# Optimization experiments

Measured on AMD Instinct MI355X. Metric: run time of the kernel, lower is better.

The kernel has to match this reference:

```python
import jax, jax.numpy as jnp
import numpy as np

N, D, H = 4096, 128, 8


def setup_inputs() -> dict:
    key = jax.random.key(0)
    ks = jax.random.split(key, 9)
    s = 1.0 / np.sqrt(D)
    return {
        "x": jax.random.normal(ks[0], (N, D), jnp.float32),
        "Wq": jax.random.normal(ks[1], (H, D, D), jnp.float32) * s,
        "bq": jax.random.normal(ks[2], (H, D), jnp.float32) * s,
        "Wk": jax.random.normal(ks[3], (H, D, D), jnp.float32) * s,
        "bk": jax.random.normal(ks[4], (H, D), jnp.float32) * s,
        "Wv": jax.random.normal(ks[5], (H, D, D), jnp.float32) * s,
        "bv": jax.random.normal(ks[6], (H, D), jnp.float32) * s,
        "Wo": jax.random.normal(ks[7], (H * D, D), jnp.float32) * s,
        "bo": jax.random.normal(ks[8], (D,), jnp.float32) * s,
    }


def reference(x, Wq, bq, Wk, bk, Wv, bv, Wo, bo):
    # Batched per-head projections: [H, N, D]
    q = jnp.einsum('nd,hde->hne', x, Wq) + bq[:, None, :]
    k = jnp.einsum('nd,hde->hne', x, Wk) + bk[:, None, :]
    v = jnp.einsum('nd,hde->hne', x, Wv) + bv[:, None, :]
    # Non-standard attention: scores = v @ q.T  -> [H, N, N]
    scores = jnp.einsum('hnd,hmd->hnm', v, q)
    wts = jax.nn.softmax(scores, axis=-1)
    out = jnp.einsum('hnm,hmd->hnd', wts, k)  # [H, N, D]
    # Concat heads along feature dim (head-major order, as torch.cat)
    outs = out.transpose(1, 0, 2).reshape(N, H * D)
    return outs @ Wo + bo
```

## Files before the change

kernel.cpp:

```cpp
#include <hip/hip_runtime.h>
#include <hip/hip_bf16.h>


typedef __attribute__((ext_vector_type(8))) short short8;
typedef __attribute__((ext_vector_type(4))) float f32x4;

#define MFMA(a,b,c) __builtin_amdgcn_mfma_f32_16x16x32_bf16((a),(b),(c),0,0,0)
#define LOG2E 1.44269504088896340736f
#define DEFER_THR 8.0f

#define AS1 __attribute__((address_space(1)))
#define AS3 __attribute__((address_space(3)))
static __device__ __forceinline__ void gld16(const void* g, void* l) {
  __builtin_amdgcn_global_load_lds((const AS1 void*)g, (AS3 void*)l, 16, 0, 0);
}

static __device__ __forceinline__ unsigned short f2bf(float f) {
  union { float f; unsigned u; } v; v.f = f;
  unsigned r = v.u + 0x7fffu + ((v.u >> 16) & 1u);
  return (unsigned short)(r >> 16);
}
static __device__ __forceinline__ float bf2f(unsigned short h) {
  union { unsigned u; float f; } v; v.u = ((unsigned)h) << 16; return v.f;
}
static __device__ __forceinline__ void split2(float f, unsigned short& hi, unsigned short& lo) {
  hi = f2bf(f);
  lo = f2bf(f - bf2f(hi));
}

__global__ __launch_bounds__(256) void kwt(const float* __restrict__ Wq,
                                           const float* __restrict__ Wk,
                                           const float* __restrict__ Wv,
                                           const float* __restrict__ Wo,
                                           unsigned short* __restrict__ WTh,
                                           unsigned short* __restrict__ WTl,
                                           unsigned short* __restrict__ WoT) {
  __shared__ float lds[64 * 130];
  int b = blockIdx.x, t = threadIdx.x;
  const float* src; int isWo;
  if (b < 24) {
    int slot = b >> 3, hh = b & 7;
    src = (slot == 0 ? Wq : (slot == 1 ? Wk : Wv)) + hh * 16384;
    isWo = 0;
  } else {
    src = Wo + (b - 24) * 16384;
    isWo = 1;
  }
  for (int half = 0; half < 2; ++half) {
#pragma unroll
    for (int i = 0; i < 8; ++i) {
      int lin = i * 1024 + t * 4;
      int row = lin >> 7, col = lin & 127;
      float4 v = *reinterpret_cast<const float4*>(src + half * 8192 + lin);
      lds[row * 130 + col + 0] = v.x;
      lds[row * 130 + col + 1] = v.y;
      lds[row * 130 + col + 2] = v.z;
      lds[row * 130 + col + 3] = v.w;
    }
    __syncthreads();
    int e = t >> 1, k0 = (t & 1) * 32;
    float buf[32];
#pragma unroll
    for (int j = 0; j < 32; ++j) buf[j] = lds[(k0 + j) * 130 + e];
    int kg = half * 64 + k0;
    if (!isWo) {
      unsigned short* dh = WTh + b * 16384 + e * 128 + kg;
      unsigned short* dl = WTl + b * 16384 + e * 128 + kg;
#pragma unroll
      for (int c = 0; c < 4; ++c) {
        short8 oh, ol;
#pragma unroll
        for (int jj = 0; jj < 8; ++jj) {
          unsigned short h, l; split2(buf[c * 8 + jj], h, l);
          oh[jj] = (short)h; ol[jj] = (short)l;
        }
        *reinterpret_cast<short8*>(dh + c * 8) = oh;
        *reinterpret_cast<short8*>(dl + c * 8) = ol;
      }
    } else {
      unsigned short* dst = WoT + e * 1024 + (b - 24) * 128 + kg;
#pragma unroll
      for (int c = 0; c < 4; ++c) {
        short8 o;
#pragma unroll
        for (int jj = 0; jj < 8; ++jj) o[jj] = (short)f2bf(buf[c * 8 + jj]);
        *reinterpret_cast<short8*>(dst + c * 8) = o;
      }
    }
    __syncthreads();
  }
}

__global__ __launch_bounds__(256) void kprojf(const float* __restrict__ x,
                                              const unsigned short* __restrict__ WThg,
                                              const unsigned short* __restrict__ WTlg,
                                              const float* __restrict__ bq,
                                              const float* __restrict__ bk,
                                              const float* __restrict__ bv,
                                              unsigned short* __restrict__ Qh,
                                              unsigned short* __restrict__ Vh,
                                              unsigned short* __restrict__ Vl,
                                              unsigned short* __restrict__ Kt) {
  __shared__ __align__(16) unsigned char lds[64 * 128 * 2];
  int nb = blockIdx.x, h = blockIdx.y;
  int t = threadIdx.x, lane = t & 63, w = t >> 6;
  int r = lane & 15, g = lane >> 4;
  int rowbase = nb * 64 + w * 16;

  short8 ah[4], al[4];
#pragma unroll
  for (int kc = 0; kc < 4; ++kc) {
    const float* xp = x + (size_t)(rowbase + r) * 128 + kc * 32 + g * 8;
    float4 f0 = *reinterpret_cast<const float4*>(xp);
    float4 f1 = *reinterpret_cast<const float4*>(xp + 4);
    unsigned short hi_, lo_;
    split2(f0.x, hi_, lo_); ah[kc][0] = (short)hi_; al[kc][0] = (short)lo_;
    split2(f0.y, hi_, lo_); ah[kc][1] = (short)hi_; al[kc][1] = (short)lo_;
    split2(f0.z, hi_, lo_); ah[kc][2] = (short)hi_; al[kc][2] = (short)lo_;
    split2(f0.w, hi_, lo_); ah[kc][3] = (short)hi_; al[kc][3] = (short)lo_;
    split2(f1.x, hi_, lo_); ah[kc][4] = (short)hi_; al[kc][4] = (short)lo_;
    split2(f1.y, hi_, lo_); ah[kc][5] = (short)hi_; al[kc][5] = (short)lo_;
    split2(f1.z, hi_, lo_); ah[kc][6] = (short)hi_; al[kc][6] = (short)lo_;
    split2(f1.w, hi_, lo_); ah[kc][7] = (short)hi_; al[kc][7] = (short)lo_;
  }

  f32x4 acc[8];
  {
    const unsigned short* Wth = WThg + (0 * 8 + h) * 16384;
    const unsigned short* Wtl = WTlg + (0 * 8 + h) * 16384;
#pragma unroll
    for (int ct = 0; ct < 8; ++ct) acc[ct] = (f32x4){0.f, 0.f, 0.f, 0.f};
#pragma unroll
    for (int ct = 0; ct < 8; ++ct) {
#pragma unroll
      for (int kc = 0; kc < 4; ++kc) {
        short8 bh = *reinterpret_cast<const short8*>(Wth + (ct * 16 + r) * 128 + kc * 32 + g * 8);
        short8 bl = *reinterpret_cast<const short8*>(Wtl + (ct * 16 + r) * 128 + kc * 32 + g * 8);
        acc[ct] = MFMA(ah[kc], bh, acc[ct]);
        acc[ct] = MFMA(ah[kc], bl, acc[ct]);
        acc[ct] = MFMA(al[kc], bh, acc[ct]);
      }
    }
    unsigned short* dh = Qh + (size_t)h * 4096 * 128;
#pragma unroll
    for (int ct = 0; ct < 8; ++ct) {
      int e = ct * 16 + r;
      float bb = bq[h * 128 + e];
#pragma unroll
      for (int rr = 0; rr < 4; ++rr) {
        int n = rowbase + g * 4 + rr;
        dh[n * 128 + e] = f2bf(acc[ct][rr] + bb);
      }
    }
  }
  {
    const unsigned short* Wth = WThg + (2 * 8 + h) * 16384;
    const unsigned short* Wtl = WTlg + (2 * 8 + h) * 16384;
#pragma unroll
    for (int ct = 0; ct < 8; ++ct) acc[ct] = (f32x4){0.f, 0.f, 0.f, 0.f};
#pragma unroll
    for (int ct = 0; ct < 8; ++ct) {
#pragma unroll
      for (int kc = 0; kc < 4; ++kc) {
        short8 bh = *reinterpret_cast<const short8*>(Wth + (ct * 16 + r) * 128 + kc * 32 + g * 8);
        short8 bl = *reinterpret_cast<const short8*>(Wtl + (ct * 16 + r) * 128 + kc * 32 + g * 8);
        acc[ct] = MFMA(ah[kc], bh, acc[ct]);
        acc[ct] = MFMA(ah[kc], bl, acc[ct]);
        acc[ct] = MFMA(al[kc], bh, acc[ct]);
      }
    }
    unsigned short* dh = Vh + (size_t)h * 4096 * 128;
    unsigned short* dl = Vl + (size_t)h * 4096 * 128;
#pragma unroll
    for (int ct = 0; ct < 8; ++ct) {
      int e = ct * 16 + r;
      float bb = bv[h * 128 + e];
#pragma unroll
      for (int rr = 0; rr < 4; ++rr) {
        int n = rowbase + g * 4 + rr;
        unsigned short hi_, lo_; split2(acc[ct][rr] + bb, hi_, lo_);
        dh[n * 128 + e] = hi_;
        dl[n * 128 + e] = lo_;
      }
    }
  }
  {
    const unsigned short* Wth = WThg + (1 * 8 + h) * 16384;
#pragma unroll
    for (int ct = 0; ct < 8; ++ct) acc[ct] = (f32x4){0.f, 0.f, 0.f, 0.f};
#pragma unroll
    for (int ct = 0; ct < 8; ++ct) {
#pragma unroll
      for (int kc = 0; kc < 4; ++kc) {
        short8 bh = *reinterpret_cast<const short8*>(Wth + (ct * 16 + r) * 128 + kc * 32 + g * 8);
        acc[ct] = MFMA(ah[kc], bh, acc[ct]);
      }
    }
#pragma unroll
    for (int ct = 0; ct < 8; ++ct) {
      int e = ct * 16 + r;
      float bb = bk[h * 128 + e];
#pragma unroll
      for (int rr = 0; rr < 4; ++rr) {
        int n = w * 16 + g * 4 + rr;
        unsigned off = ((unsigned)(n * 128 + e) * 2u) ^ ((unsigned)(n & 7) << 4);
        *reinterpret_cast<unsigned short*>(lds + off) = f2bf(acc[ct][rr] + bb);
      }
    }
    __syncthreads();
    int e = t >> 1, n0 = (t & 1) * 32;
    unsigned short buf[32];
#pragma unroll
    for (int j = 0; j < 32; ++j) {
      int n = n0 + j;
      unsigned off = ((unsigned)(n * 128 + e) * 2u) ^ ((unsigned)(n & 7) << 4);
      buf[j] = *reinterpret_cast<unsigned short*>(lds + off);
    }
    unsigned short* dst = Kt + ((size_t)h * 128 + e) * 4096 + nb * 64 + n0;
#pragma unroll
    for (int c = 0; c < 4; ++c) {
      short8 o;
#pragma unroll
      for (int jj = 0; jj < 8; ++jj) o[jj] = (short)buf[c * 8 + jj];
      *reinterpret_cast<short8*>(dst + c * 8) = o;
    }
  }
}

__global__ __launch_bounds__(128, 2) void kattn(
    const unsigned short* __restrict__ Qg,
    const unsigned short* __restrict__ Kt,
    const unsigned short* __restrict__ Vh,
    const unsigned short* __restrict__ Vl,
    unsigned short* __restrict__ Opart,
    float2* __restrict__ ml) {
  __shared__ __align__(16) unsigned char qlds[2][8192];
  __shared__ __align__(16) unsigned char klds[2][8192];
  __shared__ __align__(16) unsigned short plds[2][32 * 40];
  const int h = blockIdx.x, nb = blockIdx.y, z = blockIdx.z;
  const int t = threadIdx.x, lane = t & 63, w = t >> 6;
  const int r = lane & 15, g = lane >> 4;
  const unsigned char* Qb = (const unsigned char*)(Qg + (size_t)h * 4096 * 128);
  const unsigned char* Kb = (const unsigned char*)(Kt + (size_t)h * 128 * 4096);

  const int vbase = nb * 64 + w * 32;
  short8 va0h[4], va0l[4], va1h[4], va1l[4];
#pragma unroll
  for (int kc = 0; kc < 4; ++kc) {
    size_t o0 = (size_t)h * 4096 * 128 + (size_t)(vbase + r) * 128 + kc * 32 + g * 8;
    size_t o1 = (size_t)h * 4096 * 128 + (size_t)(vbase + 16 + r) * 128 + kc * 32 + g * 8;
    va0h[kc] = *reinterpret_cast<const short8*>(Vh + o0);
    va0l[kc] = *reinterpret_cast<const short8*>(Vl + o0);
    va1h[kc] = *reinterpret_cast<const short8*>(Vh + o1);
    va1l[kc] = *reinterpret_cast<const short8*>(Vl + o1);
  }

  f32x4 oacc0[8], oacc1[8];
#pragma unroll
  for (int dt = 0; dt < 8; ++dt) {
    oacc0[dt] = (f32x4){0.f, 0.f, 0.f, 0.f};
    oacc1[dt] = (f32x4){0.f, 0.f, 0.f, 0.f};
  }
  float m0run = -3e38f, l0run = 0.f, m1run = -3e38f, l1run = 0.f;
  const int mt0 = z * 64;

#define STAGE(buf, mtile) do {                                                   \
    const unsigned char* qsrc = Qb + (size_t)(mtile) * 8192;                     \
    const unsigned char* ksrc = Kb + (size_t)(mtile) * 64;                       \
    _Pragma("unroll")                                                            \
    for (int j = 0; j < 4; ++j) {                                                \
      int row = j * 8 + (t >> 4);                                                \
      gld16(qsrc + (size_t)row * 256 + (((unsigned)(t & 15) * 16) ^ ((unsigned)(row & 7) << 4)), \
            &qlds[buf][j * 2048 + t * 16]);                                      \
    }                                                                            \
    _Pragma("unroll")                                                            \
    for (int j = 0; j < 4; ++j) {                                                \
      int row = j * 32 + (t >> 2);                                               \
      gld16(ksrc + (size_t)row * 8192 + (unsigned)(t & 3) * 16,                  \
            &klds[buf][j * 2048 + t * 16]);                                      \
    }                                                                            \
  } while (0)

  STAGE(0, mt0);
  __syncthreads();

  const unsigned qsw = ((unsigned)(r & 7)) << 4;
  for (int it = 0; it < 64; ++it) {
    const int buf = it & 1;
    if (it < 63) STAGE(buf ^ 1, mt0 + it + 1);
    f32x4 s00 = (f32x4){0.f, 0.f, 0.f, 0.f};
    f32x4 s10 = (f32x4){0.f, 0.f, 0.f, 0.f};
    f32x4 s01 = (f32x4){0.f, 0.f, 0.f, 0.f};
    f32x4 s11 = (f32x4){0.f, 0.f, 0.f, 0.f};
    __builtin_amdgcn_s_setprio(1);
#pragma unroll
    for (int kc = 0; kc < 4; ++kc) {
      unsigned col = (unsigned)(kc * 64 + g * 16);
      short8 q0 = *reinterpret_cast<const short8*>(&qlds[buf][(unsigned)r * 256 + (col ^ qsw)]);
      short8 q1 = *reinterpret_cast<const short8*>(&qlds[buf][(unsigned)(16 + r) * 256 + (col ^ qsw)]);
      s00 = MFMA(q0, va0h[kc], s00);
      s10 = MFMA(q1, va0h[kc], s10);
      s01 = MFMA(q0, va1h[kc], s01);
      s11 = MFMA(q1, va1h[kc], s11);
      s00 = MFMA(q0, va0l[kc], s00);
      s10 = MFMA(q1, va0l[kc], s10);
      s01 = MFMA(q0, va1l[kc], s01);
      s11 = MFMA(q1, va1l[kc], s11);
    }
    __builtin_amdgcn_s_setprio(0);
    float mx0 = fmaxf(fmaxf(fmaxf(s00[0], s00[1]), fmaxf(s00[2], s00[3])),
                      fmaxf(fmaxf(s10[0], s10[1]), fmaxf(s10[2], s10[3])));
    float mx1 = fmaxf(fmaxf(fmaxf(s01[0], s01[1]), fmaxf(s01[2], s01[3])),
                      fmaxf(fmaxf(s11[0], s11[1]), fmaxf(s11[2], s11[3])));
    mx0 = fmaxf(mx0, __shfl_xor(mx0, 16)); mx0 = fmaxf(mx0, __shfl_xor(mx0, 32));
    mx1 = fmaxf(mx1, __shfl_xor(mx1, 16)); mx1 = fmaxf(mx1, __shfl_xor(mx1, 32));
    if (__any(mx0 > m0run + DEFER_THR)) {
      float nm = fmaxf(m0run, mx0);
      float sc = exp2f((m0run - nm) * LOG2E);
      l0run *= sc;
#pragma unroll
      for (int dt = 0; dt < 8; ++dt) oacc0[dt] *= sc;
      m0run = nm;
    }
    if (__any(mx1 > m1run + DEFER_THR)) {
      float nm = fmaxf(m1run, mx1);
      float sc = exp2f((m1run - nm) * LOG2E);
      l1run *= sc;
#pragma unroll
      for (int dt = 0; dt < 8; ++dt) oacc1[dt] *= sc;
      m1run = nm;
    }
    float p0[8], p1[8];
#pragma unroll
    for (int j = 0; j < 4; ++j) {
      p0[j]     = exp2f((s00[j] - m0run) * LOG2E);
      p0[4 + j] = exp2f((s10[j] - m0run) * LOG2E);
      p1[j]     = exp2f((s01[j] - m1run) * LOG2E);
      p1[4 + j] = exp2f((s11[j] - m1run) * LOG2E);
    }
    float ps0 = ((p0[0] + p0[1]) + (p0[2] + p0[3])) + ((p0[4] + p0[5]) + (p0[6] + p0[7]));
    float ps1 = ((p1[0] + p1[1]) + (p1[2] + p1[3])) + ((p1[4] + p1[5]) + (p1[6] + p1[7]));
    ps0 += __shfl_xor(ps0, 16); ps0 += __shfl_xor(ps0, 32);
    ps1 += __shfl_xor(ps1, 16); ps1 += __shfl_xor(ps1, 32);
    l0run += ps0;
    l1run += ps1;
    {
      ushort4 a, b, c, d;
      a.x = f2bf(p0[0]); a.y = f2bf(p0[1]); a.z = f2bf(p0[2]); a.w = f2bf(p0[3]);
      b.x = f2bf(p0[4]); b.y = f2bf(p0[5]); b.z = f2bf(p0[6]); b.w = f2bf(p0[7]);
      c.x = f2bf(p1[0]); c.y = f2bf(p1[1]); c.z = f2bf(p1[2]); c.w = f2bf(p1[3]);
      d.x = f2bf(p1[4]); d.y = f2bf(p1[5]); d.z = f2bf(p1[6]); d.w = f2bf(p1[7]);
      unsigned short* pw = &plds[w][0];
      *reinterpret_cast<ushort4*>(pw + r * 40 + g * 4)             = a;
      *reinterpret_cast<ushort4*>(pw + r * 40 + 16 + g * 4)        = b;
      *reinterpret_cast<ushort4*>(pw + (16 + r) * 40 + g * 4)      = c;
      *reinterpret_cast<ushort4*>(pw + (16 + r) * 40 + 16 + g * 4) = d;
    }
    short8 pa0 = *reinterpret_cast<const short8*>(&plds[w][r * 40 + g * 8]);
    short8 pa1 = *reinterpret_cast<const short8*>(&plds[w][(16 + r) * 40 + g * 8]);
    __builtin_amdgcn_s_setprio(1);
#pragma unroll
    for (int dt = 0; dt < 8; ++dt) {
      short8 kb = *reinterpret_cast<const short8*>(&klds[buf][(unsigned)(dt * 16 + r) * 64 + (unsigned)(g * 16)]);
      oacc0[dt] = MFMA(kb, pa0, oacc0[dt]);
      oacc1[dt] = MFMA(kb, pa1, oacc1[dt]);
    }
    __builtin_amdgcn_s_setprio(0);
    __syncthreads();
  }
#undef STAGE
  unsigned short* Ob = Opart + (size_t)(z * 8 + h) * 4096 * 128;
#pragma unroll
  for (int dt = 0; dt < 8; ++dt) {
#pragma unroll
    for (int rr = 0; rr < 4; ++rr) {
      int d = dt * 16 + g * 4 + rr;
      Ob[(size_t)(vbase + r) * 128 + d]      = f2bf(oacc0[dt][rr]);
      Ob[(size_t)(vbase + 16 + r) * 128 + d] = f2bf(oacc1[dt][rr]);
    }
  }
  if (g == 0) ml[(size_t)(z * 8 + h) * 4096 + vbase + r]      = make_float2(m0run, l0run);
  if (g == 1) ml[(size_t)(z * 8 + h) * 4096 + vbase + 16 + r] = make_float2(m1run, l1run);
}

__global__ __launch_bounds__(256) void koutm(const unsigned short* __restrict__ Opart,
                                             const float2* __restrict__ ml,
                                             const unsigned short* __restrict__ WoT,
                                             const float* __restrict__ bo,
                                             float* __restrict__ out) {
  int rb = blockIdx.x;
  int t = threadIdx.x, lane = t & 63, w = t >> 6;
  int r = lane & 15, g = lane >> 4;
  int row = rb * 16 + r;
  float a0[8], a1[8];
#pragma unroll
  for (int h = 0; h < 8; ++h) {
    float2 m0 = ml[(size_t)h * 4096 + row];
    float2 m1 = ml[(size_t)(8 + h) * 4096 + row];
    float M = fmaxf(m0.x, m1.x);
    float e0 = exp2f((m0.x - M) * LOG2E);
    float e1 = exp2f((m1.x - M) * LOG2E);
    float inv = 1.0f / (m0.y * e0 + m1.y * e1);
    a0[h] = e0 * inv; a1[h] = e1 * inv;
  }
  f32x4 acc0 = (f32x4){0.f, 0.f, 0.f, 0.f};
  f32x4 acc1 = (f32x4){0.f, 0.f, 0.f, 0.f};
#pragma unroll
  for (int kc = 0; kc < 32; ++kc) {
    int h = kc >> 2;
    int dof = (kc & 3) * 32 + g * 8;
    short8 o0 = *reinterpret_cast<const short8*>(Opart + ((size_t)h * 4096 + row) * 128 + dof);
    short8 o1 = *reinterpret_cast<const short8*>(Opart + ((size_t)(8 + h) * 4096 + row) * 128 + dof);
    short8 af;
#pragma unroll
    for (int j = 0; j < 8; ++j)
      af[j] = (short)f2bf(bf2f((unsigned short)o0[j]) * a0[h] +
                          bf2f((unsigned short)o1[j]) * a1[h]);
    short8 b0 = *reinterpret_cast<const short8*>(WoT + (size_t)(w * 32 + r) * 1024 + kc * 32 + g * 8);
    short8 b1 = *reinterpret_cast<const short8*>(WoT + (size_t)(w * 32 + 16 + r) * 1024 + kc * 32 + g * 8);
    acc0 = MFMA(af, b0, acc0);
    acc1 = MFMA(af, b1, acc1);
  }
#pragma unroll
  for (int rr = 0; rr < 4; ++rr) {
    int n = rb * 16 + g * 4 + rr;
    out[(size_t)n * 128 + w * 32 + r]      = acc0[rr] + bo[w * 32 + r];
    out[(size_t)n * 128 + w * 32 + 16 + r] = acc1[rr] + bo[w * 32 + 16 + r];
  }
}

extern "C" void kernel_launch(void* const* d_in, const int* in_sizes, int n_in,
                              void* d_out, int out_size, void* d_ws, size_t ws_size,
                              hipStream_t stream) {
  const float* x  = (const float*)d_in[0];
  const float* Wq = (const float*)d_in[1];
  const float* bq = (const float*)d_in[2];
  const float* Wk = (const float*)d_in[3];
  const float* bk = (const float*)d_in[4];
  const float* Wv = (const float*)d_in[5];
  const float* bv = (const float*)d_in[6];
  const float* Wo = (const float*)d_in[7];
  const float* bo = (const float*)d_in[8];
  float* out = (float*)d_out;

  unsigned short* ws = (unsigned short*)d_ws;
  unsigned short* WTh   = ws;
  unsigned short* WTl   = WTh + 393216;
  unsigned short* WoT   = WTl + 393216;
  unsigned short* Qh    = WoT + 131072;
  unsigned short* Vh    = Qh + 4194304;
  unsigned short* Vl    = Vh + 4194304;
  unsigned short* Kt    = Vl + 4194304;
  unsigned short* Opart = Kt + 4194304;
  float2*         mlp   = (float2*)(Opart + 8388608);

  kwt<<<32, 256, 0, stream>>>(Wq, Wk, Wv, Wo, WTh, WTl, WoT);
  kprojf<<<dim3(64, 8), 256, 0, stream>>>(x, WTh, WTl, bq, bk, bv, Qh, Vh, Vl, Kt);
  kattn<<<dim3(8, 64, 2), 128, 0, stream>>>(Qh, Kt, Vh, Vl, Opart, mlp);
  koutm<<<256, 256, 0, stream>>>(Opart, mlp, WoT, bo, out);
}
```

Before: 275.4 us.

## Rework attention split, register P exchange, log2 prescale, and wider kernel grids

The attention kernel now runs 256-thread blocks covering 128 query rows and splits keys four ways instead of two. The P tile is packed to bf16 and rearranged with cross-lane shuffles instead of a round trip through LDS, and the K tile in LDS is XOR-swizzled. V is pre-multiplied by log2(e) so the exponentials drop a multiply, with the deferred-rescale threshold adjusted to match. The weight-transpose and output kernels are split over more blocks, and the output kernel combines four partial results using packed bf16 conversion. The wider split adds partial-output traffic and merge work, and the raised occupancy target may increase register pressure.

```diff
diff --git a/kernel.cpp b/kernel.cpp
--- a/kernel.cpp
+++ b/kernel.cpp
@@ -7,7 +7,7 @@
 
 #define MFMA(a,b,c) __builtin_amdgcn_mfma_f32_16x16x32_bf16((a),(b),(c),0,0,0)
 #define LOG2E 1.44269504088896340736f
-#define DEFER_THR 8.0f
+#define DEFER_THR 11.5442f
 
 #define AS1 __attribute__((address_space(1)))
 #define AS3 __attribute__((address_space(3)))
@@ -26,6 +26,32 @@
 static __device__ __forceinline__ void split2(float f, unsigned short& hi, unsigned short& lo) {
   hi = f2bf(f);
   lo = f2bf(f - bf2f(hi));
+}
+static __device__ __forceinline__ unsigned cvt_pk_bf16(float lo, float hi) {
+  unsigned r;
+  asm("v_cvt_pk_bf16_f32 %0, %1, %2" : "=v"(r) : "v"(lo), "v"(hi));
+  return r;
+}
+
+static __device__ __forceinline__ void pexch(const float* p, int lane, unsigned* t) {
+  unsigned A = cvt_pk_bf16(p[0], p[1]);
+  unsigned B = cvt_pk_bf16(p[2], p[3]);
+  unsigned C = cvt_pk_bf16(p[4], p[5]);
+  unsigned D = cvt_pk_bf16(p[6], p[7]);
+  bool lo32 = (lane & 32) == 0;
+  unsigned A32 = __shfl_xor(A, 32), B32 = __shfl_xor(B, 32);
+  unsigned C32 = __shfl_xor(C, 32), D32 = __shfl_xor(D, 32);
+  unsigned u0 = lo32 ? A : C32;
+  unsigned u1 = lo32 ? A32 : C;
+  unsigned v0 = lo32 ? B : D32;
+  unsigned v1 = lo32 ? B32 : D;
+  bool eg = (lane & 16) == 0;
+  unsigned su1 = __shfl_xor(u1, 16), su0 = __shfl_xor(u0, 16);
+  unsigned sv1 = __shfl_xor(v1, 16), sv0 = __shfl_xor(v0, 16);
+  t[0] = eg ? u0 : su1;
+  t[1] = eg ? v0 : sv1;
+  t[2] = eg ? su0 : u1;
+  t[3] = eg ? sv0 : v1;
 }
 
 __global__ __launch_bounds__(256) void kwt(const float* __restrict__ Wq,
@@ -35,59 +61,53 @@
                                            unsigned short* __restrict__ WTh,
                                            unsigned short* __restrict__ WTl,
                                            unsigned short* __restrict__ WoT) {
-  __shared__ float lds[64 * 130];
+  __shared__ float lds[32 * 130];
   int b = blockIdx.x, t = threadIdx.x;
-  const float* src; int isWo;
-  if (b < 24) {
-    int slot = b >> 3, hh = b & 7;
-    src = (slot == 0 ? Wq : (slot == 1 ? Wk : Wv)) + hh * 16384;
-    isWo = 0;
+  int mat = b >> 2, q = b & 3;
+  const float* src = (mat < 8)  ? Wq + mat * 16384
+                   : (mat < 16) ? Wk + (mat - 8) * 16384
+                   : (mat < 24) ? Wv + (mat - 16) * 16384
+                                : Wo + (mat - 24) * 16384;
+  src += q * 32 * 128;
+#pragma unroll
+  for (int i = 0; i < 4; ++i) {
+    int lin = i * 1024 + t * 4;
+    int row = lin >> 7, col = lin & 127;
+    float4 v = *reinterpret_cast<const float4*>(src + lin);
+    lds[row * 130 + col + 0] = v.x;
+    lds[row * 130 + col + 1] = v.y;
+    lds[row * 130 + col + 2] = v.z;
+    lds[row * 130 + col + 3] = v.w;
+  }
+  __syncthreads();
+  int e = t >> 1, ks = (t & 1) * 16;
+  float buf[16];
+#pragma unroll
+  for (int j = 0; j < 16; ++j) buf[j] = lds[(ks + j) * 130 + e];
+  int kg = q * 32 + ks;
+  if (mat < 24) {
+    unsigned short* dh = WTh + mat * 16384 + e * 128 + kg;
+    unsigned short* dl = WTl + mat * 16384 + e * 128 + kg;
+#pragma unroll
+    for (int c = 0; c < 2; ++c) {
+      short8 oh, ol;
+#pragma unroll
+      for (int jj = 0; jj < 8; ++jj) {
+        unsigned short h, l; split2(buf[c * 8 + jj], h, l);
+        oh[jj] = (short)h; ol[jj] = (short)l;
+      }
+      *reinterpret_cast<short8*>(dh + c * 8) = oh;
+      *reinterpret_cast<short8*>(dl + c * 8) = ol;
+    }
   } else {
-    src = Wo + (b - 24) * 16384;
-    isWo = 1;
-  }
-  for (int half = 0; half < 2; ++half) {
-#pragma unroll
-    for (int i = 0; i < 8; ++i) {
-      int lin = i * 1024 + t * 4;
-      int row = lin >> 7, col = lin & 127;
-      float4 v = *reinterpret_cast<const float4*>(src + half * 8192 + lin);
-      lds[row * 130 + col + 0] = v.x;
-      lds[row * 130 + col + 1] = v.y;
-      lds[row * 130 + col + 2] = v.z;
-      lds[row * 130 + col + 3] = v.w;
-    }
-    __syncthreads();
-    int e = t >> 1, k0 = (t & 1) * 32;
-    float buf[32];
-#pragma unroll
-    for (int j = 0; j < 32; ++j) buf[j] = lds[(k0 + j) * 130 + e];
-    int kg = half * 64 + k0;
-    if (!isWo) {
-      unsigned short* dh = WTh + b * 16384 + e * 128 + kg;
-      unsigned short* dl = WTl + b * 16384 + e * 128 + kg;
-#pragma unroll
-      for (int c = 0; c < 4; ++c) {
-        short8 oh, ol;
-#pragma unroll
-        for (int jj = 0; jj < 8; ++jj) {
-          unsigned short h, l; split2(buf[c * 8 + jj], h, l);
-          oh[jj] = (short)h; ol[jj] = (short)l;
-        }
-        *reinterpret_cast<short8*>(dh + c * 8) = oh;
-        *reinterpret_cast<short8*>(dl + c * 8) = ol;
-      }
-    } else {
-      unsigned short* dst = WoT + e * 1024 + (b - 24) * 128 + kg;
-#pragma unroll
-      for (int c = 0; c < 4; ++c) {
-        short8 o;
-#pragma unroll
-        for (int jj = 0; jj < 8; ++jj) o[jj] = (short)f2bf(buf[c * 8 + jj]);
-        *reinterpret_cast<short8*>(dst + c * 8) = o;
-      }
-    }
-    __syncthreads();
+    unsigned short* dst = WoT + e * 1024 + (mat - 24) * 128 + kg;
+#pragma unroll
+    for (int c = 0; c < 2; ++c) {
+      short8 o;
+#pragma unroll
+      for (int jj = 0; jj < 8; ++jj) o[jj] = (short)f2bf(buf[c * 8 + jj]);
+      *reinterpret_cast<short8*>(dst + c * 8) = o;
+    }
   }
 }
 
@@ -178,7 +198,7 @@
 #pragma unroll
       for (int rr = 0; rr < 4; ++rr) {
         int n = rowbase + g * 4 + rr;
-        unsigned short hi_, lo_; split2(acc[ct][rr] + bb, hi_, lo_);
+        unsigned short hi_, lo_; split2((acc[ct][rr] + bb) * LOG2E, hi_, lo_);
         dh[n * 128 + e] = hi_;
         dl[n * 128 + e] = lo_;
       }
@@ -227,7 +247,7 @@
   }
 }
 
-__global__ __launch_bounds__(128, 2) void kattn(
+__global__ __launch_bounds__(256, 3) void kattn(
     const unsigned short* __restrict__ Qg,
     const unsigned short* __restrict__ Kt,
     const unsigned short* __restrict__ Vh,
@@ -236,14 +256,13 @@
     float2* __restrict__ ml) {
   __shared__ __align__(16) unsigned char qlds[2][8192];
   __shared__ __align__(16) unsigned char klds[2][8192];
-  __shared__ __align__(16) unsigned short plds[2][32 * 40];
   const int h = blockIdx.x, nb = blockIdx.y, z = blockIdx.z;
   const int t = threadIdx.x, lane = t & 63, w = t >> 6;
   const int r = lane & 15, g = lane >> 4;
   const unsigned char* Qb = (const unsigned char*)(Qg + (size_t)h * 4096 * 128);
   const unsigned char* Kb = (const unsigned char*)(Kt + (size_t)h * 128 * 4096);
 
-  const int vbase = nb * 64 + w * 32;
+  const int vbase = nb * 128 + w * 32;
   short8 va0h[4], va0l[4], va1h[4], va1l[4];
 #pragma unroll
   for (int kc = 0; kc < 4; ++kc) {
@@ -262,22 +281,23 @@
     oacc1[dt] = (f32x4){0.f, 0.f, 0.f, 0.f};
   }
   float m0run = -3e38f, l0run = 0.f, m1run = -3e38f, l1run = 0.f;
-  const int mt0 = z * 64;
+  const int mt0 = z * 32;
 
 #define STAGE(buf, mtile) do {                                                   \
     const unsigned char* qsrc = Qb + (size_t)(mtile) * 8192;                     \
     const unsigned char* ksrc = Kb + (size_t)(mtile) * 64;                       \
     _Pragma("unroll")                                                            \
-    for (int j = 0; j < 4; ++j) {                                                \
-      int row = j * 8 + (t >> 4);                                                \
+    for (int j = 0; j < 2; ++j) {                                                \
+      int row = j * 16 + (t >> 4);                                               \
       gld16(qsrc + (size_t)row * 256 + (((unsigned)(t & 15) * 16) ^ ((unsigned)(row & 7) << 4)), \
-            &qlds[buf][j * 2048 + t * 16]);                                      \
+            &qlds[buf][j * 4096 + t * 16]);                                      \
     }                                                                            \
     _Pragma("unroll")                                                            \
-    for (int j = 0; j < 4; ++j) {                                                \
-      int row = j * 32 + (t >> 2);                                               \
-      gld16(ksrc + (size_t)row * 8192 + (unsigned)(t & 3) * 16,                  \
-            &klds[buf][j * 2048 + t * 16]);                                      \
+    for (int j = 0; j < 2; ++j) {                                                \
+      int d = j * 64 + (t >> 2);                                                 \
+      int c = (t & 3) ^ (d & 3);                                                 \
+      gld16(ksrc + (size_t)d * 8192 + (unsigned)c * 16,                          \
+            &klds[buf][j * 4096 + t * 16]);                                      \
     }                                                                            \
   } while (0)
 
@@ -285,9 +305,10 @@
   __syncthreads();
 
   const unsigned qsw = ((unsigned)(r & 7)) << 4;
-  for (int it = 0; it < 64; ++it) {
+  const unsigned kxor = ((unsigned)(g ^ (r & 3))) << 4;
+  for (int it = 0; it < 32; ++it) {
     const int buf = it & 1;
-    if (it < 63) STAGE(buf ^ 1, mt0 + it + 1);
+    if (it < 31) STAGE(buf ^ 1, mt0 + it + 1);
     f32x4 s00 = (f32x4){0.f, 0.f, 0.f, 0.f};
     f32x4 s10 = (f32x4){0.f, 0.f, 0.f, 0.f};
     f32x4 s01 = (f32x4){0.f, 0.f, 0.f, 0.f};
@@ -316,7 +337,7 @@
     mx1 = fmaxf(mx1, __shfl_xor(mx1, 16)); mx1 = fmaxf(mx1, __shfl_xor(mx1, 32));
     if (__any(mx0 > m0run + DEFER_THR)) {
       float nm = fmaxf(m0run, mx0);
-      float sc = exp2f((m0run - nm) * LOG2E);
+      float sc = exp2f(m0run - nm);
       l0run *= sc;
 #pragma unroll
       for (int dt = 0; dt < 8; ++dt) oacc0[dt] *= sc;
@@ -324,7 +345,7 @@
     }
     if (__any(mx1 > m1run + DEFER_THR)) {
       float nm = fmaxf(m1run, mx1);
-      float sc = exp2f((m1run - nm) * LOG2E);
+      float sc = exp2f(m1run - nm);
       l1run *= sc;
 #pragma unroll
       for (int dt = 0; dt < 8; ++dt) oacc1[dt] *= sc;
@@ -333,10 +354,10 @@
     float p0[8], p1[8];
 #pragma unroll
     for (int j = 0; j < 4; ++j) {
-      p0[j]     = exp2f((s00[j] - m0run) * LOG2E);
-      p0[4 + j] = exp2f((s10[j] - m0run) * LOG2E);
-      p1[j]     = exp2f((s01[j] - m1run) * LOG2E);
-      p1[4 + j] = exp2f((s11[j] - m1run) * LOG2E);
+      p0[j]     = exp2f(s00[j] - m0run);
+      p0[4 + j] = exp2f(s10[j] - m0run);
+      p1[j]     = exp2f(s01[j] - m1run);
+      p1[4 + j] = exp2f(s11[j] - m1run);
     }
     float ps0 = ((p0[0] + p0[1]) + (p0[2] + p0[3])) + ((p0[4] + p0[5]) + (p0[6] + p0[7]));
     float ps1 = ((p1[0] + p1[1]) + (p1[2] + p1[3])) + ((p1[4] + p1[5]) + (p1[6] + p1[7]));
@@ -344,26 +365,16 @@
     ps1 += __shfl_xor(ps1, 16); ps1 += __shfl_xor(ps1, 32);
     l0run += ps0;
     l1run += ps1;
-    {
-      ushort4 a, b, c, d;
-      a.x = f2bf(p0[0]); a.y = f2bf(p0[1]); a.z = f2bf(p0[2]); a.w = f2bf(p0[3]);
-      b.x = f2bf(p0[4]); b.y = f2bf(p0[5]); b.z = f2bf(p0[6]); b.w = f2bf(p0[7]);
-      c.x = f2bf(p1[0]); c.y = f2bf(p1[1]); c.z = f2bf(p1[2]); c.w = f2bf(p1[3]);
-      d.x = f2bf(p1[4]); d.y = f2bf(p1[5]); d.z = f2bf(p1[6]); d.w = f2bf(p1[7]);
-      unsigned short* pw = &plds[w][0];
-      *reinterpret_cast<ushort4*>(pw + r * 40 + g * 4)             = a;
-      *reinterpret_cast<ushort4*>(pw + r * 40 + 16 + g * 4)        = b;
-      *reinterpret_cast<ushort4*>(pw + (16 + r) * 40 + g * 4)      = c;
-      *reinterpret_cast<ushort4*>(pw + (16 + r) * 40 + 16 + g * 4) = d;
-    }
-    short8 pa0 = *reinterpret_cast<const short8*>(&plds[w][r * 40 + g * 8]);
-    short8 pa1 = *reinterpret_cast<const short8*>(&plds[w][(16 + r) * 40 + g * 8]);
+    union { unsigned u[4]; short8 s8; } pa0u, pa1u;
+    pexch(p0, lane, pa0u.u);
+    pexch(p1, lane, pa1u.u);
     __builtin_amdgcn_s_setprio(1);
 #pragma unroll
     for (int dt = 0; dt < 8; ++dt) {
-      short8 kb = *reinterpret_cast<const short8*>(&klds[buf][(unsigned)(dt * 16 + r) * 64 + (unsigned)(g * 16)]);
-      oacc0[dt] = MFMA(kb, pa0, oacc0[dt]);
-      oacc1[dt] = MFMA(kb, pa1, oacc1[dt]);
+      short8 kb = *reinterpret_cast<const short8*>(
+          &klds[buf][((unsigned)(dt * 16 + r) * 64) + kxor]);
+      oacc0[dt] = MFMA(kb, pa0u.s8, oacc0[dt]);
+      oacc1[dt] = MFMA(kb, pa1u.s8, oacc1[dt]);
     }
     __builtin_amdgcn_s_setprio(0);
     __syncthreads();
@@ -388,44 +399,51 @@
                                              const unsigned short* __restrict__ WoT,
                                              const float* __restrict__ bo,
                                              float* __restrict__ out) {
-  int rb = blockIdx.x;
+  int rb = blockIdx.x, ch = blockIdx.y;
   int t = threadIdx.x, lane = t & 63, w = t >> 6;
   int r = lane & 15, g = lane >> 4;
   int row = rb * 16 + r;
-  float a0[8], a1[8];
+  float a[4][8];
 #pragma unroll
   for (int h = 0; h < 8; ++h) {
-    float2 m0 = ml[(size_t)h * 4096 + row];
-    float2 m1 = ml[(size_t)(8 + h) * 4096 + row];
-    float M = fmaxf(m0.x, m1.x);
-    float e0 = exp2f((m0.x - M) * LOG2E);
-    float e1 = exp2f((m1.x - M) * LOG2E);
-    float inv = 1.0f / (m0.y * e0 + m1.y * e1);
-    a0[h] = e0 * inv; a1[h] = e1 * inv;
-  }
-  f32x4 acc0 = (f32x4){0.f, 0.f, 0.f, 0.f};
-  f32x4 acc1 = (f32x4){0.f, 0.f, 0.f, 0.f};
+    float2 m0 = ml[(size_t)(0 * 8 + h) * 4096 + row];
+    float2 m1 = ml[(size_t)(1 * 8 + h) * 4096 + row];
+    float2 m2 = ml[(size_t)(2 * 8 + h) * 4096 + row];
+    float2 m3 = ml[(size_t)(3 * 8 + h) * 4096 + row];
+    float M = fmaxf(fmaxf(m0.x, m1.x), fmaxf(m2.x, m3.x));
+    float e0 = exp2f(m0.x - M), e1 = exp2f(m1.x - M);
+    float e2 = exp2f(m2.x - M), e3 = exp2f(m3.x - M);
+    float inv = 1.0f / (m0.y * e0 + m1.y * e1 + m2.y * e2 + m3.y * e3);
+    a[0][h] = e0 * inv; a[1][h] = e1 * inv; a[2][h] = e2 * inv; a[3][h] = e3 * inv;
+  }
+  int e0c = ch * 64 + w * 16;
+  f32x4 acc = (f32x4){0.f, 0.f, 0.f, 0.f};
 #pragma unroll
   for (int kc = 0; kc < 32; ++kc) {
     int h = kc >> 2;
     int dof = (kc & 3) * 32 + g * 8;
-    short8 o0 = *reinterpret_cast<const short8*>(Opart + ((size_t)h * 4096 + row) * 128 + dof);
-    short8 o1 = *reinterpret_cast<const short8*>(Opart + ((size_t)(8 + h) * 4096 + row) * 128 + dof);
-    short8 af;
-#pragma unroll
-    for (int j = 0; j < 8; ++j)
-      af[j] = (short)f2bf(bf2f((unsigned short)o0[j]) * a0[h] +
-                          bf2f((unsigned short)o1[j]) * a1[h]);
-    short8 b0 = *reinterpret_cast<const short8*>(WoT + (size_t)(w * 32 + r) * 1024 + kc * 32 + g * 8);
-    short8 b1 = *reinterpret_cast<const short8*>(WoT + (size_t)(w * 32 + 16 + r) * 1024 + kc * 32 + g * 8);
-    acc0 = MFMA(af, b0, acc0);
-    acc1 = MFMA(af, b1, acc1);
-  }
+    float af[8];
+#pragma unroll
+    for (int j = 0; j < 8; ++j) af[j] = 0.f;
+#pragma unroll
+    for (int zz = 0; zz < 4; ++zz) {
+      short8 o = *reinterpret_cast<const short8*>(
+          Opart + ((size_t)(zz * 8 + h) * 4096 + row) * 128 + dof);
+      float az = a[zz][h];
+#pragma unroll
+      for (int j = 0; j < 8; ++j) af[j] += bf2f((unsigned short)o[j]) * az;
+    }
+    union { unsigned u[4]; short8 s8; } afp;
+#pragma unroll
+    for (int j = 0; j < 4; ++j) afp.u[j] = cvt_pk_bf16(af[2 * j], af[2 * j + 1]);
+    short8 b0 = *reinterpret_cast<const short8*>(WoT + (size_t)(e0c + r) * 1024 + kc * 32 + g * 8);
+    acc = MFMA(afp.s8, b0, acc);
+  }
+  float bov = bo[e0c + r];
 #pragma unroll
   for (int rr = 0; rr < 4; ++rr) {
     int n = rb * 16 + g * 4 + rr;
-    out[(size_t)n * 128 + w * 32 + r]      = acc0[rr] + bo[w * 32 + r];
-    out[(size_t)n * 128 + w * 32 + 16 + r] = acc1[rr] + bo[w * 32 + 16 + r];
+    out[(size_t)n * 128 + e0c + r] = acc[rr] + bov;
   }
 }
 
@@ -452,10 +470,10 @@
   unsigned short* Vl    = Vh + 4194304;
   unsigned short* Kt    = Vl + 4194304;
   unsigned short* Opart = Kt + 4194304;
-  float2*         mlp   = (float2*)(Opart + 8388608);
-
-  kwt<<<32, 256, 0, stream>>>(Wq, Wk, Wv, Wo, WTh, WTl, WoT);
+  float2*         mlp   = (float2*)(Opart + 16777216);
+
+  kwt<<<128, 256, 0, stream>>>(Wq, Wk, Wv, Wo, WTh, WTl, WoT);
   kprojf<<<dim3(64, 8), 256, 0, stream>>>(x, WTh, WTl, bq, bk, bv, Qh, Vh, Vl, Kt);
-  kattn<<<dim3(8, 64, 2), 128, 0, stream>>>(Qh, Kt, Vh, Vl, Opart, mlp);
-  koutm<<<256, 256, 0, stream>>>(Opart, mlp, WoT, bo, out);
-}
+  kattn<<<dim3(8, 32, 4), 256, 0, stream>>>(Qh, Kt, Vh, Vl, Opart, mlp);
+  koutm<<<dim3(256, 2), 256, 0, stream>>>(Opart, mlp, WoT, bo, out);
+}
```

Result: slower. 328.4 us (+19.3%).
